# Kernel optimization log

Hardware: AMD Instinct MI355X
Metric: run time of the kernel (lower is better)

Reference implementation:

```python
import jax, jax.numpy as jnp
import numpy as np
from jax import lax

IDIM, CDIM, N, M = 512, 512, 1024, 64
T, BSZ = 256, 128


def setup_inputs() -> dict:
    key = jax.random.key(0)
    ks = jax.random.split(key, 16)
    s = 5.0 / np.sqrt(IDIM + M + CDIM)  # controller init range from _reset_controller
    f32 = jnp.float32
    inp = {
        "embs": jax.random.normal(ks[0], (T, BSZ, IDIM), f32),
        # LSTM controller params (PyTorch layout, gate order i,f,g,o)
        "w_ih": jax.random.uniform(ks[1], (4 * CDIM, IDIM + M), f32, -s, s),
        "w_hh": jax.random.uniform(ks[2], (4 * CDIM, CDIM), f32, -s, s),
        "b_ih": jnp.zeros((4 * CDIM,), f32),
        "b_hh": jnp.zeros((4 * CDIM,), f32),
        # initial states
        "h0": jax.random.normal(ks[3], (CDIM,), f32) * 0.05,
        "c0": jax.random.normal(ks[4], (CDIM,), f32) * 0.05,
        "r0": jax.random.normal(ks[5], (M,), f32) * 0.02,
        "mem0": jax.random.normal(ks[6], (N, M), f32) * 0.05,
        # NTM-style addressing heads (concrete read/write instantiation)
        "W_rk": jax.random.normal(ks[7], (M, CDIM), f32) / np.sqrt(CDIM),
        "b_rk": jnp.zeros((M,), f32),
        "W_wk": jax.random.normal(ks[8], (M, CDIM), f32) / np.sqrt(CDIM),
        "b_wk": jnp.zeros((M,), f32),
        "W_e": jax.random.normal(ks[9], (M, CDIM), f32) / np.sqrt(CDIM),
        "b_e": jnp.zeros((M,), f32),
        "W_a": jax.random.normal(ks[10], (M, IDIM), f32) / np.sqrt(IDIM),
        "b_a": jnp.zeros((M,), f32),
    }
    return inp


def reference(embs, w_ih, w_hh, b_ih, b_hh, h0, c0, r0, mem0,
              W_rk, b_rk, W_wk, b_wk, W_e, b_e, W_a, b_a):
    bsz = embs.shape[1]
    b = b_ih + b_hh
    h = jnp.broadcast_to(h0, (bsz, CDIM))
    c = jnp.broadcast_to(c0, (bsz, CDIM))
    r = jnp.broadcast_to(r0, (bsz, M))
    mem = jnp.broadcast_to(mem0, (bsz, N, M))

    def step(carry, emb):
        h, c, r, mem = carry
        # LSTM controller step on [emb, r]
        x = jnp.concatenate([emb, r], axis=-1)          # [bsz, idim+M]
        gates = x @ w_ih.T + h @ w_hh.T + b             # [bsz, 4*cdim]
        i, f, g, o = jnp.split(gates, 4, axis=-1)
        i = jax.nn.sigmoid(i)
        f = jax.nn.sigmoid(f)
        g = jnp.tanh(g)
        o = jax.nn.sigmoid(o)
        c_new = f * c + i * g
        h_new = o * jnp.tanh(c_new)                     # controller_outp == h (1-layer LSTM)
        # read_first=True: content-based read, then erase/add write
        k_r = h_new @ W_rk.T + b_rk                     # [bsz, M]
        w_r = jax.nn.softmax(jnp.einsum('bnm,bm->bn', mem, k_r), axis=-1)
        r_new = jnp.einsum('bn,bnm->bm', w_r, mem)      # [bsz, M]
        k_w = h_new @ W_wk.T + b_wk
        w_w = jax.nn.softmax(jnp.einsum('bnm,bm->bn', mem, k_w), axis=-1)
        e = jax.nn.sigmoid(h_new @ W_e.T + b_e)         # erase vector [bsz, M]
        a = jnp.tanh(emb @ W_a.T + b_a)                 # add vector from input emb
        mem_new = mem * (1.0 - w_w[:, :, None] * e[:, None, :]) + w_w[:, :, None] * a[:, None, :]
        out = jnp.concatenate([h_new, r_new], axis=-1)  # [bsz, cdim+M]
        return (h_new, c_new, r_new, mem_new), out

    _, os = lax.scan(step, (h, c, r, mem), embs)
    return os  # [T, bsz, cdim+M]
```

## Files before the change

### kernel.cpp

```cpp
#include <hip/hip_runtime.h>


#define T_STEPS 256
#define BSZ     128
#define IDIM    512
#define CDIM    512
#define MW      64
#define G4      2048
#define ODIM    576

typedef unsigned short u16;
typedef unsigned int   u32;
typedef short  short8  __attribute__((ext_vector_type(8)));
typedef float  floatx4 __attribute__((ext_vector_type(4)));
typedef float  f4      __attribute__((ext_vector_type(4)));

__device__ __forceinline__ float bf2f(u16 h){ return __uint_as_float(((u32)h)<<16); }
__device__ __forceinline__ u16   f2bf(float f){ u32 u = __float_as_uint(f); return (u16)((u + 0x7fffu + ((u>>16)&1u))>>16); }
__device__ __forceinline__ float sigm(float x){ return 1.f/(1.f+__expf(-x)); }

__device__ __forceinline__ f4 vld4(const float* p){ return *(const volatile f4*)p; }
__device__ __forceinline__ float vldf(const float* p){ return *(const volatile float*)p; }
__device__ __forceinline__ void vstf(float* p, float v){ *(volatile float*)p = v; }
__device__ __forceinline__ void vst4(float* p, f4 v){ *(volatile f4*)p = v; }

__device__ __forceinline__ void flag_set(u32* p, u32 v){
    __hip_atomic_store(p, v, __ATOMIC_RELAXED, __HIP_MEMORY_SCOPE_AGENT);
}
__device__ __forceinline__ void flag_wait(u32* p, u32 v){
    while (__hip_atomic_load(p, __ATOMIC_RELAXED, __HIP_MEMORY_SCOPE_AGENT) < v)
        __builtin_amdgcn_s_sleep(2);
}
#define VMDRAIN() asm volatile("s_waitcnt vmcnt(0)" ::: "memory")
#define CBAR()    asm volatile("" ::: "memory")


__global__ void prep_wt(const float* __restrict__ wih, const float* __restrict__ whh,
                        const float* __restrict__ bih, const float* __restrict__ bhh,
                        u16* __restrict__ WT, float* __restrict__ biasp){
    int idx = blockIdx.x*256 + threadIdx.x;
    if (idx >= 136*G4) return;
    int j  = idx & (G4-1);
    int kg = idx >> 11;
    int ro = (j&3)*512 + (j>>2);
    u32 ohi[4], olo[4];
    #pragma unroll
    for (int p=0;p<4;p++){
        int k0 = kg*8 + p*2;
        float v0 = (k0   < 576) ? wih[ro*576 + k0  ] : whh[ro*512 + k0   - 576];
        float v1 = (k0+1 < 576) ? wih[ro*576 + k0+1] : whh[ro*512 + k0+1 - 576];
        u16 h0b = f2bf(v0), h1b = f2bf(v1);
        u16 l0b = f2bf(v0 - bf2f(h0b)), l1b = f2bf(v1 - bf2f(h1b));
        ohi[p] = (u32)h0b | ((u32)h1b<<16);
        olo[p] = (u32)l0b | ((u32)l1b<<16);
    }
    *(uint4*)&WT[(size_t)idx*16]     = make_uint4(ohi[0],ohi[1],ohi[2],ohi[3]);
    *(uint4*)&WT[(size_t)idx*16 + 8] = make_uint4(olo[0],olo[1],olo[2],olo[3]);
    if (idx < G4) biasp[j] = bih[ro] + bhh[ro];
}

__global__ void prep_misc(const float* __restrict__ Wrk, const float* __restrict__ Wwk,
                          const float* __restrict__ We,  const float* __restrict__ Wa,
                          const float* __restrict__ brk, const float* __restrict__ bwk,
                          const float* __restrict__ be,  const float* __restrict__ ba,
                          const float* __restrict__ h0,  const float* __restrict__ r0,
                          u16* __restrict__ Wk, float* __restrict__ kb,
                          float* __restrict__ hbuf, float* __restrict__ xr,
                          u32* __restrict__ hflag, u32* __restrict__ rflag){
    int idx = blockIdx.x*256 + threadIdx.x;
    if (idx < 32768) {
        int d4 = idx >> 8, k = idx & 255;
        const float* src = (k<64)? Wrk + k*512 : (k<128)? Wwk + (k-64)*512
                         : (k<192)? We + (k-128)*512 : Wa + (k-192)*512;
        u32 a = (u32)f2bf(src[d4*4+0]) | ((u32)f2bf(src[d4*4+1])<<16);
        u32 b = (u32)f2bf(src[d4*4+2]) | ((u32)f2bf(src[d4*4+3])<<16);
        *(uint2*)&Wk[(size_t)idx*4] = make_uint2(a,b);
    } else if (idx < 33024) {
        int k = idx - 32768;
        kb[k] = (k<64)? brk[k] : (k<128)? bwk[k-64] : (k<192)? be[k-128] : ba[k-192];
    } else if (idx < 98560) {
        int i = idx - 33024;
        hbuf[65536 + i] = h0[i & 511];
    } else if (idx < 106752) {
        int i = idx - 98560;
        xr[i] = r0[i & 63];
    } else if (idx < 108800) {
        hflag[idx - 106752] = 0u;
    } else if (idx < 110848) {
        rflag[idx - 108800] = 0u;
    }
}


__device__ __forceinline__ short8 pack_hi(f4 a, f4 b){
    union { short8 s; u16 u[8]; } r;
    r.u[0]=f2bf(a[0]); r.u[1]=f2bf(a[1]); r.u[2]=f2bf(a[2]); r.u[3]=f2bf(a[3]);
    r.u[4]=f2bf(b[0]); r.u[5]=f2bf(b[1]); r.u[6]=f2bf(b[2]); r.u[7]=f2bf(b[3]);
    return r.s;
}
__device__ __forceinline__ void pack_hilo(f4 a, f4 b, short8& hh, short8& ll){
    union { short8 s; u16 u[8]; } H, L;
    float v[8] = {a[0],a[1],a[2],a[3],b[0],b[1],b[2],b[3]};
    #pragma unroll
    for (int i=0;i<8;i++){ u16 hb = f2bf(v[i]); H.u[i]=hb; L.u[i]=f2bf(v[i]-bf2f(hb)); }
    hh = H.s; ll = L.s;
}

__device__ __forceinline__ void blkMax2(float& va, float& vb, float* red){
    #pragma unroll
    for (int o=32;o;o>>=1){ va = fmaxf(va, __shfl_xor(va,o,64)); vb = fmaxf(vb, __shfl_xor(vb,o,64)); }
    int wv = threadIdx.x >> 6;
    if ((threadIdx.x & 63) == 0){ red[wv] = va; red[8+wv] = vb; }
    __syncthreads();
    float ra = red[0], rb = red[8];
    #pragma unroll
    for (int i=1;i<8;i++){ ra = fmaxf(ra, red[i]); rb = fmaxf(rb, red[8+i]); }
    va = ra; vb = rb;
}
__device__ __forceinline__ void blkSum2(float& va, float& vb, float* red){
    #pragma unroll
    for (int o=32;o;o>>=1){ va += __shfl_xor(va,o,64); vb += __shfl_xor(vb,o,64); }
    int wv = threadIdx.x >> 6;
    if ((threadIdx.x & 63) == 0){ red[wv] = va; red[8+wv] = vb; }
    __syncthreads();
    float ra = red[0], rb = red[8];
    #pragma unroll
    for (int i=1;i<8;i++){ ra += red[i]; rb += red[8+i]; }
    va = ra; vb = rb;
}

__device__ __forceinline__ float key_gemv(const float* src, const u16* __restrict__ Wk,
                                          int key, int d0){
    const uint2* wp = (const uint2*)Wk;
    float a0=0.f, a1=0.f, a2=0.f, a3=0.f;
    #pragma unroll 8
    for (int dd = 0; dd < 256; dd += 4) {
        uint2 wv2 = wp[((d0+dd)>>2)*256 + key];
        a0 += src[d0+dd+0]*bf2f((u16)(wv2.x & 0xffffu));
        a1 += src[d0+dd+1]*bf2f((u16)(wv2.x >> 16));
        a2 += src[d0+dd+2]*bf2f((u16)(wv2.y & 0xffffu));
        a3 += src[d0+dd+3]*bf2f((u16)(wv2.y >> 16));
    }
    return (a0+a1)+(a2+a3);
}

#define BSTEP ((size_t)(4*G4*16))

__device__ __forceinline__ void emb_part1(floatx4& acc, const float* embrow,
                                          const u16* __restrict__ bp0){
    acc[0]=0.f; acc[1]=0.f; acc[2]=0.f; acc[3]=0.f;
    #pragma unroll 2
    for (int ks = 0; ks < 16; ++ks) {
        f4 e0 = *(const f4*)(embrow + ks*32);
        f4 e1 = *(const f4*)(embrow + ks*32 + 4);
        short8 af = pack_hi(e0, e1);
        const u16* bks = bp0 + (size_t)ks*BSTEP;
        short8 bh = *(const short8*)(bks);
        short8 bl = *(const short8*)(bks + 8);
        acc = __builtin_amdgcn_mfma_f32_16x16x32_bf16(af, bh, acc, 0,0,0);
        acc = __builtin_amdgcn_mfma_f32_16x16x32_bf16(af, bl, acc, 0,0,0);
    }
}

__launch_bounds__(512)
__global__ void mann_persist(const float* __restrict__ embs, const u16* __restrict__ WT,
                             const float* __restrict__ biasp, const u16* __restrict__ Wk,
                             const float* __restrict__ kbias,
                             float* __restrict__ hbuf, float* __restrict__ xr,
                             const float* __restrict__ mem0, const float* __restrict__ c0,
                             float* __restrict__ out,
                             u32* __restrict__ hflag, u32* __restrict__ rflag){
    __shared__ __align__(16) char smraw[140800];
    float* sp = (float*)smraw;
    const int w = blockIdx.x;
    const int tid = threadIdx.x;
    if (w >= 256) return;

    if (w < 128) {
        float* part = sp;
        float* gsc  = sp + 33280;
        float* keys = sp + 33792;
        float* red  = sp + 34048;
        float* hb   = sp + 34080;
        float* ebb  = sp + 34592;
        const int b = w;
        const int key = tid & 255, kh = tid >> 8, d0 = kh*256;
        const int n0 = tid*2;

        float m0[64], m1[64];
        #pragma unroll
        for (int m4=0;m4<16;m4++){
            f4 v0 = *(const f4*)(mem0 + (size_t)n0*64 + m4*4);
            f4 v1 = *(const f4*)(mem0 + (size_t)(n0+1)*64 + m4*4);
            #pragma unroll
            for (int j=0;j<4;j++){ m0[m4*4+j] = v0[j]; m1[m4*4+j] = v1[j]; }
        }

        ebb[tid] = embs[(size_t)b*IDIM + tid];
        __syncthreads();
        if (key >= 192) gsc[tid] = key_gemv(ebb, Wk, key, d0);

        for (int t = 0; t < T_STEPS; ++t) {
            if (tid < 16) flag_wait(&hflag[((b>>4)*16 + tid)*16], (u32)(t+1));
            __syncthreads();
            CBAR();
            hb[tid] = vldf(hbuf + (t&1)*65536 + b*CDIM + tid);
            __syncthreads();
            if (key < 192) gsc[tid] = key_gemv(hb, Wk, key, d0);
            __syncthreads();
            if (tid < 256) {
                float acc = kbias[tid] + gsc[tid] + gsc[tid+256];
                if (tid >= 192)      acc = tanhf(acc);
                else if (tid >= 128) acc = sigm(acc);
                keys[tid] = acc;
            }
            __syncthreads();

            float s0r=0.f, s0w=0.f, s1r=0.f, s1w=0.f;
            #pragma unroll
            for (int m4=0;m4<16;m4++){
                f4 kr = *(const f4*)&keys[m4*4];
                f4 kw = *(const f4*)&keys[64 + m4*4];
                #pragma unroll
                for (int j=0;j<4;j++){
                    s0r += m0[m4*4+j]*kr[j]; s1r += m1[m4*4+j]*kr[j];
                    s0w += m0[m4*4+j]*kw[j]; s1w += m1[m4*4+j]*kw[j];
                }
            }
            float Mr = fmaxf(s0r, s1r), Mw = fmaxf(s0w, s1w);
            blkMax2(Mr, Mw, red);
            float e0r = __expf(s0r - Mr), e1r = __expf(s1r - Mr);
            float e0w = __expf(s0w - Mw), e1w = __expf(s1w - Mw);
            float Sr = e0r + e1r, Sw = e0w + e1w;
            blkSum2(Sr, Sw, red + 16);

            float* prow = part + tid*65;
            #pragma unroll
            for (int m=0;m<64;m++) prow[m] = e0r*m0[m] + e1r*m1[m];
            __syncthreads();
            {
                int mm = tid & 63, blk = tid >> 6;
                const float* pb2 = part + (size_t)blk*64*65 + mm;
                float s = 0.f;
                #pragma unroll
                for (int r=0;r<64;r++) s += pb2[r*65];
                gsc[tid] = s;
            }
            __syncthreads();
            float rv = 0.f;
            if (tid < 64) {
                #pragma unroll
                for (int k=0;k<8;k++) rv += gsc[k*64 + tid];
                rv /= Sr;
                vstf(xr + b*MW + tid, rv);
            }
            VMDRAIN();
            if (tid == 0) flag_set(&rflag[b*16], (u32)(t+1));

            if (tid < 64)
                out[((size_t)(t*BSZ + b))*ODIM + 512 + tid] = rv;
            float iSw = 1.f / Sw;
            float w0 = e0w*iSw, w1 = e1w*iSw;
            #pragma unroll
            for (int m4=0;m4<16;m4++){
                f4 ev = *(const f4*)&keys[128 + m4*4];
                f4 av = *(const f4*)&keys[192 + m4*4];
                #pragma unroll
                for (int j=0;j<4;j++){
                    m0[m4*4+j] = m0[m4*4+j]*(1.f - w0*ev[j]) + w0*av[j];
                    m1[m4*4+j] = m1[m4*4+j]*(1.f - w1*ev[j]) + w1*av[j];
                }
            }
            if (t + 1 < T_STEPS) {
                ebb[tid] = embs[((size_t)((t+1)*BSZ + b))*IDIM + tid];
                __syncthreads();
                if (key >= 192) gsc[tid] = key_gemv(ebb, Wk, key, d0);
            }
        }
    } else {
        float* hst  = sp;
        float* hst2 = sp + 8256;
        const int a = w - 128, bgrp = a >> 4, cseg = a & 15;
        const int lane = tid & 63, wv = tid >> 6, jl = lane & 15, q = lane >> 4;
        const int jcol = cseg*128 + wv*16 + jl;
        const int gl = jl & 3;
        const u16* bp0 = WT + ((size_t)q*G4 + jcol)*16;

        const float bias = biasp[jcol];
        float creg[4];
        {
            float cv = c0[jcol >> 2];
            creg[0]=cv; creg[1]=cv; creg[2]=cv; creg[3]=cv;
        }
        floatx4 acc;
        emb_part1(acc, embs + (size_t)(bgrp*16 + jl)*IDIM + q*8, bp0);

        for (int t = 0; t < T_STEPS; ++t) {
            if (tid < 16) flag_wait(&hflag[(bgrp*16 + tid)*16], (u32)t);
            __syncthreads();
            CBAR();
            {
                const float* hsrc = hbuf + ((t+1)&1)*65536 + (size_t)bgrp*16*CDIM;
                #pragma unroll
                for (int p=0;p<4;p++){
                    int idx = p*2048 + tid*4;
                    f4 v = vld4(hsrc + idx);
                    *(f4*)&hst[(idx>>9)*516 + (idx&511)] = v;
                }
            }
            __syncthreads();
            #pragma unroll 2
            for (int ks = 18; ks < 34; ++ks) {
                int d = (ks-18)*32 + q*8;
                f4 h0v = *(const f4*)&hst[jl*516 + d];
                f4 h1v = *(const f4*)&hst[jl*516 + d + 4];
                short8 ah, al; pack_hilo(h0v, h1v, ah, al);
                const u16* bks = bp0 + (size_t)ks*BSTEP;
                short8 bh = *(const short8*)(bks);
                short8 bl = *(const short8*)(bks + 8);
                acc = __builtin_amdgcn_mfma_f32_16x16x32_bf16(ah, bh, acc, 0,0,0);
                acc = __builtin_amdgcn_mfma_f32_16x16x32_bf16(al, bh, acc, 0,0,0);
                acc = __builtin_amdgcn_mfma_f32_16x16x32_bf16(ah, bl, acc, 0,0,0);
            }

            if (tid < 16) flag_wait(&rflag[(bgrp*16 + tid)*16], (u32)t);
            __syncthreads();
            CBAR();
            #pragma unroll
            for (int ks = 16; ks < 18; ++ks) {
                const float* rr = xr + (size_t)(bgrp*16 + jl)*MW + (ks-16)*32 + q*8;
                f4 r0v = vld4(rr);
                f4 r1v = vld4(rr + 4);
                short8 ah, al; pack_hilo(r0v, r1v, ah, al);
                const u16* bks = bp0 + (size_t)ks*BSTEP;
                short8 bh = *(const short8*)(bks);
                short8 bl = *(const short8*)(bks + 8);
                acc = __builtin_amdgcn_mfma_f32_16x16x32_bf16(ah, bh, acc, 0,0,0);
                acc = __builtin_amdgcn_mfma_f32_16x16x32_bf16(al, bh, acc, 0,0,0);
                acc = __builtin_amdgcn_mfma_f32_16x16x32_bf16(ah, bl, acc, 0,0,0);
            }
            #pragma unroll
            for (int rg = 0; rg < 4; ++rg) {
                float gval = acc[rg] + bias;
                float tval = (gl == 2) ? tanhf(gval) : sigm(gval);
                int base = lane & ~3;
                float iv = __shfl(tval, base+0, 64);
                float fv = __shfl(tval, base+1, 64);
                float gv = __shfl(tval, base+2, 64);
                float ov = __shfl(tval, base+3, 64);
                if (gl == 0) {
                    float cn = fv*creg[rg] + iv*gv;
                    creg[rg] = cn;
                    float hn = ov*tanhf(cn);
                    int nloc = wv*4 + (jl >> 2);
                    hst2[(q*4+rg)*32 + nloc] = hn;
                }
            }
            __syncthreads();
            if (tid < 128) {
                float* hw = hbuf + (t&1)*65536;
                int idx = tid*4;
                int brl = tid >> 3, nloc = idx & 31;
                f4 v = *(const f4*)&hst2[brl*32 + nloc];
                vst4(hw + (size_t)(bgrp*16 + brl)*CDIM + cseg*32 + nloc, v);
            }
            VMDRAIN();
            __syncthreads();
            if (tid == 0) flag_set(&hflag[a*16], (u32)(t+1));

            if (tid < 128) {
                int idx = tid*4;
                int brl = tid >> 3, nloc = idx & 31;
                f4 v = *(const f4*)&hst2[brl*32 + nloc];
                *(f4*)(out + ((size_t)(t*BSZ + bgrp*16 + brl))*ODIM + cseg*32 + nloc) = v;
            }
            if (t + 1 < T_STEPS)
                emb_part1(acc, embs + ((size_t)((t+1)*BSZ + bgrp*16 + jl))*IDIM + q*8, bp0);
        }
    }
}


#define OFF_WT     0u
#define OFF_BIASP  8912896u
#define OFF_WK     8921088u
#define OFF_KBIAS  9183232u
#define OFF_HBUF   9184256u
#define OFF_XR     9708544u
#define OFF_HFLAG  9741312u
#define OFF_RFLAG  9749504u
#define WS_NEED    9901056u

extern "C" void kernel_launch(void* const* d_in, const int* in_sizes, int n_in,
                              void* d_out, int out_size, void* d_ws, size_t ws_size,
                              hipStream_t stream) {
    if (ws_size < (size_t)WS_NEED) return;

    const float* embs = (const float*)d_in[0];
    const float* w_ih = (const float*)d_in[1];
    const float* w_hh = (const float*)d_in[2];
    const float* b_ih = (const float*)d_in[3];
    const float* b_hh = (const float*)d_in[4];
    const float* h0   = (const float*)d_in[5];
    const float* c0   = (const float*)d_in[6];
    const float* r0   = (const float*)d_in[7];
    const float* mem0 = (const float*)d_in[8];
    const float* Wrk  = (const float*)d_in[9];
    const float* brk  = (const float*)d_in[10];
    const float* Wwk  = (const float*)d_in[11];
    const float* bwk  = (const float*)d_in[12];
    const float* We   = (const float*)d_in[13];
    const float* be   = (const float*)d_in[14];
    const float* Wa   = (const float*)d_in[15];
    const float* ba   = (const float*)d_in[16];

    char* ws = (char*)d_ws;
    u16*   WT    = (u16*)  (ws + OFF_WT);
    float* biasp = (float*)(ws + OFF_BIASP);
    u16*   Wk    = (u16*)  (ws + OFF_WK);
    float* kbias = (float*)(ws + OFF_KBIAS);
    float* hbuf  = (float*)(ws + OFF_HBUF);
    float* xrp   = (float*)(ws + OFF_XR);
    u32*   hflag = (u32*)  (ws + OFF_HFLAG);
    u32*   rflag = (u32*)  (ws + OFF_RFLAG);
    float* outp  = (float*)d_out;

    hipLaunchKernelGGL(prep_wt,   dim3(1088), dim3(256), 0, stream,
                       w_ih, w_hh, b_ih, b_hh, WT, biasp);
    hipLaunchKernelGGL(prep_misc, dim3(512),  dim3(256), 0, stream,
                       Wrk, Wwk, We, Wa, brk, bwk, be, ba, h0, r0,
                       Wk, kbias, hbuf, xrp, hflag, rflag);

    const float* embs_c = embs; const u16* WT_c = WT; const float* biasp_c = biasp;
    const u16* Wk_c = Wk; const float* kbias_c = kbias;
    const float* mem0_c = mem0; const float* c0_c = c0;
    void* kargs[] = { (void*)&embs_c, (void*)&WT_c, (void*)&biasp_c, (void*)&Wk_c,
                      (void*)&kbias_c, (void*)&hbuf, (void*)&xrp, (void*)&mem0_c,
                      (void*)&c0_c, (void*)&outp, (void*)&hflag, (void*)&rflag };
    hipLaunchCooperativeKernel((void*)mann_persist, dim3(256), dim3(512), kargs, 0, stream);
}
```

Baseline: 6.401 ms.

## Move LSTM cell nonlinearities from gate-GEMM blocks into per-batch memory blocks

The gate-GEMM blocks now publish raw pre-activation gates (with bias folded into the accumulator init) to a global buffer and signal a new flag. The per-batch memory blocks read these gates, apply the LSTM cell update with c held in a register, and write h to the h buffer and the output. This removes the shuffle-based cell math from the GEMM critical path and lets the memory block start its key GEMV right after computing h. It costs an extra global round-trip of the 2048-wide gate vector per batch row, plus an additional flag handshake per step. The spin-wait sleep is also shortened.

```diff
diff --git a/kernel.cpp b/kernel.cpp
--- a/kernel.cpp
+++ b/kernel.cpp
@@ -29,7 +29,7 @@
 }
 __device__ __forceinline__ void flag_wait(u32* p, u32 v){
     while (__hip_atomic_load(p, __ATOMIC_RELAXED, __HIP_MEMORY_SCOPE_AGENT) < v)
-        __builtin_amdgcn_s_sleep(2);
+        __builtin_amdgcn_s_sleep(1);
 }
 #define VMDRAIN() asm volatile("s_waitcnt vmcnt(0)" ::: "memory")
 #define CBAR()    asm volatile("" ::: "memory")
@@ -66,7 +66,8 @@
                           const float* __restrict__ h0,  const float* __restrict__ r0,
                           u16* __restrict__ Wk, float* __restrict__ kb,
                           float* __restrict__ hbuf, float* __restrict__ xr,
-                          u32* __restrict__ hflag, u32* __restrict__ rflag){
+                          u32* __restrict__ hflag, u32* __restrict__ rflag,
+                          u32* __restrict__ pflag){
     int idx = blockIdx.x*256 + threadIdx.x;
     if (idx < 32768) {
         int d4 = idx >> 8, k = idx & 255;
@@ -88,6 +89,8 @@
         hflag[idx - 106752] = 0u;
     } else if (idx < 110848) {
         rflag[idx - 108800] = 0u;
+    } else if (idx < 112896) {
+        pflag[idx - 110848] = 0u;
     }
 }
 
@@ -147,8 +150,8 @@
 #define BSTEP ((size_t)(4*G4*16))
 
 __device__ __forceinline__ void emb_part1(floatx4& acc, const float* embrow,
-                                          const u16* __restrict__ bp0){
-    acc[0]=0.f; acc[1]=0.f; acc[2]=0.f; acc[3]=0.f;
+                                          const u16* __restrict__ bp0, float bias){
+    acc[0]=bias; acc[1]=bias; acc[2]=bias; acc[3]=bias;
     #pragma unroll 2
     for (int ks = 0; ks < 16; ++ks) {
         f4 e0 = *(const f4*)(embrow + ks*32);
@@ -167,9 +170,11 @@
                              const float* __restrict__ biasp, const u16* __restrict__ Wk,
                              const float* __restrict__ kbias,
                              float* __restrict__ hbuf, float* __restrict__ xr,
+                             float* __restrict__ Apart,
                              const float* __restrict__ mem0, const float* __restrict__ c0,
                              float* __restrict__ out,
-                             u32* __restrict__ hflag, u32* __restrict__ rflag){
+                             u32* __restrict__ hflag, u32* __restrict__ rflag,
+                             u32* __restrict__ pflag){
     __shared__ __align__(16) char smraw[140800];
     float* sp = (float*)smraw;
     const int w = blockIdx.x;
@@ -177,12 +182,12 @@
     if (w >= 256) return;
 
     if (w < 128) {
-        float* part = sp;
-        float* gsc  = sp + 33280;
-        float* keys = sp + 33792;
-        float* red  = sp + 34048;
-        float* hb   = sp + 34080;
-        float* ebb  = sp + 34592;
+        float* part  = sp;
+        float* gsc   = sp + 33280;
+        float* keys  = sp + 33792;
+        float* red   = sp + 34048;
+        float* h_lds = sp + 34080;
+        float* ebb   = sp + 34592;
         const int b = w;
         const int key = tid & 255, kh = tid >> 8, d0 = kh*256;
         const int n0 = tid*2;
@@ -195,24 +200,37 @@
             #pragma unroll
             for (int j=0;j<4;j++){ m0[m4*4+j] = v0[j]; m1[m4*4+j] = v1[j]; }
         }
+        float c = c0[tid];
 
         ebb[tid] = embs[(size_t)b*IDIM + tid];
         __syncthreads();
         if (key >= 192) gsc[tid] = key_gemv(ebb, Wk, key, d0);
 
         for (int t = 0; t < T_STEPS; ++t) {
-            if (tid < 16) flag_wait(&hflag[((b>>4)*16 + tid)*16], (u32)(t+1));
+            if (tid < 16) flag_wait(&pflag[((b>>4)*16 + tid)*16], (u32)(t+1));
             __syncthreads();
             CBAR();
-            hb[tid] = vldf(hbuf + (t&1)*65536 + b*CDIM + tid);
-            __syncthreads();
-            if (key < 192) gsc[tid] = key_gemv(hb, Wk, key, d0);
+            f4 g4 = vld4(Apart + (size_t)b*G4 + tid*4);
+            c = sigm(g4[1])*c + sigm(g4[0])*tanhf(g4[2]);
+            float hn = sigm(g4[3])*tanhf(c);
+            h_lds[tid] = hn;
+            __syncthreads();
+            if (tid < 128)
+                vst4(hbuf + (t&1)*65536 + (size_t)b*CDIM + tid*4,
+                     *(const f4*)&h_lds[tid*4]);
+            VMDRAIN();
+            __syncthreads();
+            if (tid == 0) flag_set(&hflag[b*16], (u32)(t+1));
+
+            if (tid < 128)
+                *(f4*)(out + ((size_t)(t*BSZ + b))*ODIM + tid*4) = *(const f4*)&h_lds[tid*4];
+            if (key < 192) gsc[tid] = key_gemv(h_lds, Wk, key, d0);
             __syncthreads();
             if (tid < 256) {
-                float acc = kbias[tid] + gsc[tid] + gsc[tid+256];
-                if (tid >= 192)      acc = tanhf(acc);
-                else if (tid >= 128) acc = sigm(acc);
-                keys[tid] = acc;
+                float kv = kbias[tid] + gsc[tid] + gsc[tid+256];
+                if (tid >= 192)      kv = tanhf(kv);
+                else if (tid >= 128) kv = sigm(kv);
+                keys[tid] = kv;
             }
             __syncthreads();
 
@@ -279,21 +297,15 @@
         }
     } else {
         float* hst  = sp;
-        float* hst2 = sp + 8256;
+        float* Apl  = sp + 8256;
         const int a = w - 128, bgrp = a >> 4, cseg = a & 15;
         const int lane = tid & 63, wv = tid >> 6, jl = lane & 15, q = lane >> 4;
         const int jcol = cseg*128 + wv*16 + jl;
-        const int gl = jl & 3;
         const u16* bp0 = WT + ((size_t)q*G4 + jcol)*16;
-
         const float bias = biasp[jcol];
-        float creg[4];
-        {
-            float cv = c0[jcol >> 2];
-            creg[0]=cv; creg[1]=cv; creg[2]=cv; creg[3]=cv;
-        }
+
         floatx4 acc;
-        emb_part1(acc, embs + (size_t)(bgrp*16 + jl)*IDIM + q*8, bp0);
+        emb_part1(acc, embs + (size_t)(bgrp*16 + jl)*IDIM + q*8, bp0, bias);
 
         for (int t = 0; t < T_STEPS; ++t) {
             if (tid < 16) flag_wait(&hflag[(bgrp*16 + tid)*16], (u32)t);
@@ -340,42 +352,21 @@
                 acc = __builtin_amdgcn_mfma_f32_16x16x32_bf16(ah, bl, acc, 0,0,0);
             }
             #pragma unroll
-            for (int rg = 0; rg < 4; ++rg) {
-                float gval = acc[rg] + bias;
-                float tval = (gl == 2) ? tanhf(gval) : sigm(gval);
-                int base = lane & ~3;
-                float iv = __shfl(tval, base+0, 64);
-                float fv = __shfl(tval, base+1, 64);
-                float gv = __shfl(tval, base+2, 64);
-                float ov = __shfl(tval, base+3, 64);
-                if (gl == 0) {
-                    float cn = fv*creg[rg] + iv*gv;
-                    creg[rg] = cn;
-                    float hn = ov*tanhf(cn);
-                    int nloc = wv*4 + (jl >> 2);
-                    hst2[(q*4+rg)*32 + nloc] = hn;
-                }
-            }
-            __syncthreads();
-            if (tid < 128) {
-                float* hw = hbuf + (t&1)*65536;
-                int idx = tid*4;
-                int brl = tid >> 3, nloc = idx & 31;
-                f4 v = *(const f4*)&hst2[brl*32 + nloc];
-                vst4(hw + (size_t)(bgrp*16 + brl)*CDIM + cseg*32 + nloc, v);
+            for (int rg = 0; rg < 4; ++rg)
+                Apl[(q*4+rg)*132 + wv*16 + jl] = acc[rg];
+            __syncthreads();
+            {
+                int row = tid >> 5, c4 = (tid & 31)*4;
+                f4 v = *(const f4*)&Apl[row*132 + c4];
+                vst4(Apart + (size_t)(bgrp*16 + row)*G4 + cseg*128 + c4, v);
             }
             VMDRAIN();
             __syncthreads();
-            if (tid == 0) flag_set(&hflag[a*16], (u32)(t+1));
-
-            if (tid < 128) {
-                int idx = tid*4;
-                int brl = tid >> 3, nloc = idx & 31;
-                f4 v = *(const f4*)&hst2[brl*32 + nloc];
-                *(f4*)(out + ((size_t)(t*BSZ + bgrp*16 + brl))*ODIM + cseg*32 + nloc) = v;
-            }
+            if (tid == 0) flag_set(&pflag[a*16], (u32)(t+1));
+
             if (t + 1 < T_STEPS)
-                emb_part1(acc, embs + ((size_t)((t+1)*BSZ + bgrp*16 + jl))*IDIM + q*8, bp0);
+                emb_part1(acc, embs + ((size_t)((t+1)*BSZ + bgrp*16 + jl))*IDIM + q*8,
+                          bp0, bias);
         }
     }
 }
@@ -387,9 +378,11 @@
 #define OFF_KBIAS  9183232u
 #define OFF_HBUF   9184256u
 #define OFF_XR     9708544u
-#define OFF_HFLAG  9741312u
-#define OFF_RFLAG  9749504u
-#define WS_NEED    9901056u
+#define OFF_APART  9741312u
+#define OFF_HFLAG  10789888u
+#define OFF_RFLAG  10798080u
+#define OFF_PFLAG  10806272u
+#define WS_NEED    10814464u
 
 extern "C" void kernel_launch(void* const* d_in, const int* in_sizes, int n_in,
                               void* d_out, int out_size, void* d_ws, size_t ws_size,
@@ -421,21 +414,24 @@
     float* kbias = (float*)(ws + OFF_KBIAS);
     float* hbuf  = (float*)(ws + OFF_HBUF);
     float* xrp   = (float*)(ws + OFF_XR);
+    float* Apart = (float*)(ws + OFF_APART);
     u32*   hflag = (u32*)  (ws + OFF_HFLAG);
     u32*   rflag = (u32*)  (ws + OFF_RFLAG);
+    u32*   pflag = (u32*)  (ws + OFF_PFLAG);
     float* outp  = (float*)d_out;
 
     hipLaunchKernelGGL(prep_wt,   dim3(1088), dim3(256), 0, stream,
                        w_ih, w_hh, b_ih, b_hh, WT, biasp);
     hipLaunchKernelGGL(prep_misc, dim3(512),  dim3(256), 0, stream,
                        Wrk, Wwk, We, Wa, brk, bwk, be, ba, h0, r0,
-                       Wk, kbias, hbuf, xrp, hflag, rflag);
+                       Wk, kbias, hbuf, xrp, hflag, rflag, pflag);
 
     const float* embs_c = embs; const u16* WT_c = WT; const float* biasp_c = biasp;
     const u16* Wk_c = Wk; const float* kbias_c = kbias;
     const float* mem0_c = mem0; const float* c0_c = c0;
     void* kargs[] = { (void*)&embs_c, (void*)&WT_c, (void*)&biasp_c, (void*)&Wk_c,
-                      (void*)&kbias_c, (void*)&hbuf, (void*)&xrp, (void*)&mem0_c,
-                      (void*)&c0_c, (void*)&outp, (void*)&hflag, (void*)&rflag };
+                      (void*)&kbias_c, (void*)&hbuf, (void*)&xrp, (void*)&Apart,
+                      (void*)&mem0_c, (void*)&c0_c, (void*)&outp,
+                      (void*)&hflag, (void*)&rflag, (void*)&pflag };
     hipLaunchCooperativeKernel((void*)mann_persist, dim3(256), dim3(512), kargs, 0, stream);
 }
```

Result: slower. 8.105 ms (+26.6%).
